# Kernel optimization log

Hardware: AMD Instinct MI355X
Metric: run time of the kernel (lower is better)

## Reference

```python
import jax, jax.numpy as jnp
import numpy as np

N_NODES = 100000


def setup_inputs() -> dict:
    key = jax.random.key(0)
    k1, k2, k3, k4, k5 = jax.random.split(key, 5)
    in_dim, out_dim, n_edges = 128, 128, 640000
    x = jax.random.normal(k1, (N_NODES, in_dim), dtype=jnp.float32)
    src = jax.random.randint(k2, (n_edges,), 0, N_NODES, dtype=jnp.int32)
    dst = jax.random.randint(k3, (n_edges,), 0, N_NODES, dtype=jnp.int32)
    edge_index = jnp.stack([src, dst], axis=0)  # [2, E]
    # nn.Linear default init: U(-1/sqrt(in_dim), 1/sqrt(in_dim))
    bound = 1.0 / np.sqrt(in_dim)
    W = jax.random.uniform(k4, (out_dim, in_dim), minval=-bound, maxval=bound, dtype=jnp.float32)
    b = jax.random.uniform(k5, (out_dim,), minval=-bound, maxval=bound, dtype=jnp.float32)
    return {"x": x, "edge_index": edge_index, "W": W, "b": b}


def reference(x, edge_index, W, b):
    src, dst = edge_index[0], edge_index[1]
    # scatter-sum of gathered source features into destination nodes
    agg = jax.ops.segment_sum(x[src], dst, num_segments=N_NODES)       # [N, d]
    deg = jax.ops.segment_sum(jnp.ones((src.shape[0], 1), x.dtype), dst,
                              num_segments=N_NODES)                     # [N, 1]
    deg = jnp.maximum(deg, 1.0)
    h = agg / deg + x                                                   # mean-agg + residual
    out = jax.nn.relu(h @ W.T + b)                                      # linear + relu (dropout p=0)
    return out
```

## Files before the change

### kernel.cpp

```cpp
#include <hip/hip_runtime.h>
#include <hip/hip_bf16.h>

constexpr int N_NODES = 100000;
constexpr int DIM     = 128;
constexpr int N_EDGES = 640000;

constexpr int CHUNK     = 1024;
constexpr int N_CHUNKS  = (N_NODES + CHUNK - 1) / CHUNK;
constexpr int BINCAP    = 8192;
constexpr int EPB       = 1024;
constexpr int SRC_BITS  = 17;
constexpr int SRC_MASK  = (1 << SRC_BITS) - 1;

constexpr int YNB = 32;

typedef __attribute__((ext_vector_type(4))) float        f32x4;
typedef __attribute__((ext_vector_type(8))) short        bf16x8;
typedef __attribute__((ext_vector_type(4))) unsigned int u32x4;

static __device__ inline unsigned short f2bf(float f) {
    __hip_bfloat16 h = __float2bfloat16(f);
    return *reinterpret_cast<unsigned short*>(&h);
}
static __device__ inline float bf_lo(unsigned u) { return __uint_as_float(u << 16); }
static __device__ inline float bf_hi(unsigned u) { return __uint_as_float(u & 0xffff0000u); }

static __device__ inline bf16x8 pack8(f32x4 a, f32x4 b) {
    bf16x8 v;
    v[0] = (short)f2bf(a.x); v[1] = (short)f2bf(a.y);
    v[2] = (short)f2bf(a.z); v[3] = (short)f2bf(a.w);
    v[4] = (short)f2bf(b.x); v[5] = (short)f2bf(b.y);
    v[6] = (short)f2bf(b.z); v[7] = (short)f2bf(b.w);
    return v;
}

__global__ __launch_bounds__(256) void gcn_gemm_y(
    const float* __restrict__ x,
    const float* __restrict__ W,
    unsigned short* __restrict__ y,
    int* __restrict__ bincur)
{
    __shared__ unsigned short wl[DIM][DIM + 8];

    const int tid = threadIdx.x;
    const int n0  = blockIdx.x * YNB;

    if (blockIdx.x == 0 && tid < 128) bincur[tid] = 0;

    #pragma unroll
    for (int rep = 0; rep < 8; ++rep) {
        const int e   = rep * 2048 + tid * 8;
        const int row = e >> 7;
        const int col = e & 127;
        f32x4 a = *reinterpret_cast<const f32x4*>(W + e);
        f32x4 b = *reinterpret_cast<const f32x4*>(W + e + 4);
        *reinterpret_cast<bf16x8*>(&wl[row][col]) = pack8(a, b);
    }
    __syncthreads();

    const int w    = tid >> 6;
    const int lane = tid & 63;
    const int r    = lane & 15;
    const int g    = lane >> 4;
    const int rowt  = w & 1;
    const int cbase = 4 * (w >> 1);

    bf16x8 af[4];
    #pragma unroll
    for (int t = 0; t < 4; ++t) {
        const float* xp = x + (size_t)(n0 + 16 * rowt + r) * DIM + 32 * t + 8 * g;
        f32x4 a = *reinterpret_cast<const f32x4*>(xp);
        f32x4 b = *reinterpret_cast<const f32x4*>(xp + 4);
        af[t] = pack8(a, b);
    }

    #pragma unroll
    for (int cc = 0; cc < 4; ++cc) {
        const int c = cbase + cc;
        f32x4 acc = {0.f, 0.f, 0.f, 0.f};
        #pragma unroll
        for (int t = 0; t < 4; ++t) {
            bf16x8 wf = *reinterpret_cast<const bf16x8*>(&wl[16 * c + r][32 * t + 8 * g]);
            acc = __builtin_amdgcn_mfma_f32_16x16x32_bf16(af[t], wf, acc, 0, 0, 0);
        }
        #pragma unroll
        for (int q = 0; q < 4; ++q)
            y[(size_t)(n0 + 16 * rowt + 4 * g + q) * DIM + 16 * c + r] =
                f2bf(acc[q]);
    }
}

__global__ __launch_bounds__(256) void gcn_bin(const int* __restrict__ src,
                                               const int* __restrict__ dst,
                                               int* __restrict__ bincur,
                                               unsigned int* __restrict__ bindata)
{
    __shared__ int bh[N_CHUNKS];
    __shared__ int btb[N_CHUNKS];

    const int t  = threadIdx.x;
    const int e0 = blockIdx.x * EPB + t * 4;

    if (t < N_CHUNKS) bh[t] = 0;
    __syncthreads();

    const int4 s4 = *reinterpret_cast<const int4*>(src + e0);
    const int4 d4 = *reinterpret_cast<const int4*>(dst + e0);

    int bin[4], pos[4];
    unsigned pv[4];
    const int ds[4] = {d4.x, d4.y, d4.z, d4.w};
    const int ss[4] = {s4.x, s4.y, s4.z, s4.w};
    #pragma unroll
    for (int q = 0; q < 4; ++q) {
        bin[q] = ds[q] >> 10;
        pv[q]  = (unsigned)ss[q] | ((unsigned)(ds[q] & (CHUNK - 1)) << SRC_BITS);
        pos[q] = atomicAdd(&bh[bin[q]], 1);
    }
    __syncthreads();

    if (t < N_CHUNKS) btb[t] = atomicAdd(&bincur[t], bh[t]);
    __syncthreads();

    #pragma unroll
    for (int q = 0; q < 4; ++q)
        bindata[(size_t)bin[q] * BINCAP + btb[bin[q]] + pos[q]] = pv[q];
}

__global__ __launch_bounds__(256) void gcn_build(const int* __restrict__ bincur,
                                                 unsigned int* __restrict__ bindata,
                                                 int* __restrict__ off)
{
    __shared__ unsigned stage[BINCAP];
    __shared__ int hist[CHUNK];
    __shared__ int s[256];

    const int c  = blockIdx.x;
    const int t  = threadIdx.x;
    const int nb = min(bincur[c], BINCAP);
    unsigned int* region = bindata + (size_t)c * BINCAP;

    for (int e = t; e < nb; e += 256) stage[e] = region[e];
    #pragma unroll
    for (int q = 0; q < 4; ++q) hist[t + 256 * q] = 0;
    __syncthreads();

    for (int e = t; e < nb; e += 256)
        atomicAdd(&hist[stage[e] >> SRC_BITS], 1);
    __syncthreads();

    int h0 = hist[4 * t + 0], h1 = hist[4 * t + 1];
    int h2 = hist[4 * t + 2], h3 = hist[4 * t + 3];
    s[t] = h0 + h1 + h2 + h3;
    __syncthreads();
    for (int d = 1; d < 256; d <<= 1) {
        int add = (t >= d) ? s[t - d] : 0;
        __syncthreads();
        s[t] += add;
        __syncthreads();
    }
    int excl = (t > 0) ? s[t - 1] : 0;

    const int st0 = excl;
    const int st1 = excl + h0;
    const int st2 = excl + h0 + h1;
    const int st3 = excl + h0 + h1 + h2;
    hist[4 * t + 0] = st0;  hist[4 * t + 1] = st1;
    hist[4 * t + 2] = st2;  hist[4 * t + 3] = st3;

    const int nbase = c * CHUNK;
    if (nbase + 4 * t + 0 < N_NODES) off[nbase + 4 * t + 0] = st0 | (h0 << 13);
    if (nbase + 4 * t + 1 < N_NODES) off[nbase + 4 * t + 1] = st1 | (h1 << 13);
    if (nbase + 4 * t + 2 < N_NODES) off[nbase + 4 * t + 2] = st2 | (h2 << 13);
    if (nbase + 4 * t + 3 < N_NODES) off[nbase + 4 * t + 3] = st3 | (h3 << 13);
    __syncthreads();

    for (int e = t; e < nb; e += 256) {
        unsigned v  = stage[e];
        int slot    = atomicAdd(&hist[v >> SRC_BITS], 1);
        region[slot] = v & SRC_MASK;
    }
}

static __device__ inline void acc8(float* acc, u32x4 v) {
    #pragma unroll
    for (int q = 0; q < 4; ++q) {
        unsigned u = v[q];
        acc[2 * q]     += bf_lo(u);
        acc[2 * q + 1] += bf_hi(u);
    }
}

__global__ __launch_bounds__(256) void gcn_agg(
    const unsigned short* __restrict__ y,
    const int* __restrict__ off,
    const unsigned int* __restrict__ csr,
    const float* __restrict__ bias,
    float* __restrict__ out)
{
    const int tid    = threadIdx.x;
    const int lane16 = tid & 15;
    const int n      = blockIdx.x * 16 + (tid >> 4);
    const int col8   = lane16 * 8;

    const int meta  = off[n];
    const int count = meta >> 13;
    int i           = (n >> 10) * BINCAP + (meta & (BINCAP - 1));
    const int end   = i + count;

    float acc[8];
    #pragma unroll
    for (int q = 0; q < 8; ++q) acc[q] = 0.0f;

    for (; i + 4 <= end; i += 4) {
        int s0 = csr[i], s1 = csr[i + 1], s2 = csr[i + 2], s3 = csr[i + 3];
        u32x4 v0 = *reinterpret_cast<const u32x4*>(y + (size_t)s0 * DIM + col8);
        u32x4 v1 = *reinterpret_cast<const u32x4*>(y + (size_t)s1 * DIM + col8);
        u32x4 v2 = *reinterpret_cast<const u32x4*>(y + (size_t)s2 * DIM + col8);
        u32x4 v3 = *reinterpret_cast<const u32x4*>(y + (size_t)s3 * DIM + col8);
        acc8(acc, v0); acc8(acc, v1); acc8(acc, v2); acc8(acc, v3);
    }
    for (; i < end; ++i) {
        u32x4 v = *reinterpret_cast<const u32x4*>(y + (size_t)csr[i] * DIM + col8);
        acc8(acc, v);
    }

    const float inv = 1.0f / fmaxf((float)count, 1.0f);
    const u32x4 yr = *reinterpret_cast<const u32x4*>(y + (size_t)n * DIM + col8);
    const f32x4 b0 = *reinterpret_cast<const f32x4*>(bias + col8);
    const f32x4 b1 = *reinterpret_cast<const f32x4*>(bias + col8 + 4);

    f32x4 o0, o1;
    o0.x = fmaxf(acc[0] * inv + bf_lo(yr[0]) + b0.x, 0.0f);
    o0.y = fmaxf(acc[1] * inv + bf_hi(yr[0]) + b0.y, 0.0f);
    o0.z = fmaxf(acc[2] * inv + bf_lo(yr[1]) + b0.z, 0.0f);
    o0.w = fmaxf(acc[3] * inv + bf_hi(yr[1]) + b0.w, 0.0f);
    o1.x = fmaxf(acc[4] * inv + bf_lo(yr[2]) + b1.x, 0.0f);
    o1.y = fmaxf(acc[5] * inv + bf_hi(yr[2]) + b1.y, 0.0f);
    o1.z = fmaxf(acc[6] * inv + bf_lo(yr[3]) + b1.z, 0.0f);
    o1.w = fmaxf(acc[7] * inv + bf_hi(yr[3]) + b1.w, 0.0f);

    *reinterpret_cast<f32x4*>(out + (size_t)n * DIM + col8)     = o0;
    *reinterpret_cast<f32x4*>(out + (size_t)n * DIM + col8 + 4) = o1;
}

extern "C" void kernel_launch(void* const* d_in, const int* in_sizes, int n_in,
                              void* d_out, int out_size, void* d_ws, size_t ws_size,
                              hipStream_t stream)
{
    const float* x    = (const float*)d_in[0];
    const int*   eidx = (const int*)d_in[1];
    const float* W    = (const float*)d_in[2];
    const float* bias = (const float*)d_in[3];
    float*       out  = (float*)d_out;

    const int* src = eidx;
    const int* dst = eidx + N_EDGES;

    int* bincur = (int*)d_ws;
    int* off    = bincur + 128;
    unsigned int* bindata = (unsigned int*)(off + 100352);
    unsigned short* y = (unsigned short*)(bindata + (size_t)N_CHUNKS * BINCAP);

    gcn_gemm_y<<<N_NODES / YNB, 256, 0, stream>>>(x, W, y, bincur);
    gcn_bin   <<<N_EDGES / EPB, 256, 0, stream>>>(src, dst, bincur, bindata);
    gcn_build <<<N_CHUNKS, 256, 0, stream>>>(bincur, bindata, off);
    gcn_agg   <<<N_NODES / 16, 256, 0, stream>>>(y, off, bindata, bias, out);
}
```

Baseline: 90.85 us.

## Fuse edge binning into GEMM launch and replace global bin atomics with per-block counts

The edge-binning kernel is merged into the GEMM kernel as extra blocks, which removes one launch and lets binning overlap the matrix multiply. Instead of global atomic bin cursors, each bin block writes its edges locally sorted by chunk and records per-chunk counts and offsets. The build kernel prefix-sums those counts and gathers each chunk's edges serially per thread into shared memory. Output stores become nontemporal. The serial per-thread gather in build loads up to about 30 small segments per thread and may be poorly balanced and uncoalesced.

```diff
diff --git a/kernel.cpp b/kernel.cpp
--- a/kernel.cpp
+++ b/kernel.cpp
@@ -12,7 +12,10 @@
 constexpr int SRC_BITS  = 17;
 constexpr int SRC_MASK  = (1 << SRC_BITS) - 1;
 
-constexpr int YNB = 32;
+constexpr int YNB         = 32;
+constexpr int GEMM_BLOCKS = N_NODES / YNB;
+constexpr int BIN_BLOCKS  = N_EDGES / EPB;
+constexpr int DSTRIDE     = 640;
 
 typedef __attribute__((ext_vector_type(4))) float        f32x4;
 typedef __attribute__((ext_vector_type(8))) short        bf16x8;
@@ -34,18 +37,68 @@
     return v;
 }
 
-__global__ __launch_bounds__(256) void gcn_gemm_y(
+__global__ __launch_bounds__(256) void gcn_gemm_bin(
     const float* __restrict__ x,
     const float* __restrict__ W,
+    const int* __restrict__ esrc,
+    const int* __restrict__ edst,
     unsigned short* __restrict__ y,
-    int* __restrict__ bincur)
+    unsigned int* __restrict__ blkdata,
+    int* __restrict__ bcnt,
+    int* __restrict__ bst)
 {
     __shared__ unsigned short wl[DIM][DIM + 8];
+    __shared__ int bh[N_CHUNKS];
+    __shared__ int bpre[128];
 
     const int tid = threadIdx.x;
-    const int n0  = blockIdx.x * YNB;
-
-    if (blockIdx.x == 0 && tid < 128) bincur[tid] = 0;
+
+    if (blockIdx.x >= GEMM_BLOCKS) {
+        const int b  = blockIdx.x - GEMM_BLOCKS;
+        const int e0 = b * EPB + tid * 4;
+
+        if (tid < N_CHUNKS) bh[tid] = 0;
+        __syncthreads();
+
+        const int4 s4 = *reinterpret_cast<const int4*>(esrc + e0);
+        const int4 d4 = *reinterpret_cast<const int4*>(edst + e0);
+        const int ds[4] = {d4.x, d4.y, d4.z, d4.w};
+        const int ss[4] = {s4.x, s4.y, s4.z, s4.w};
+
+        int bin[4], pos[4];
+        unsigned pv[4];
+        #pragma unroll
+        for (int q = 0; q < 4; ++q) {
+            bin[q] = ds[q] >> 10;
+            pv[q]  = (unsigned)ss[q] | ((unsigned)(ds[q] & (CHUNK - 1)) << SRC_BITS);
+            pos[q] = atomicAdd(&bh[bin[q]], 1);
+        }
+        __syncthreads();
+
+        if (tid < 128) bpre[tid] = (tid < N_CHUNKS) ? bh[tid] : 0;
+        __syncthreads();
+        for (int d = 1; d < 128; d <<= 1) {
+            int add = 0;
+            if (tid < 128 && tid >= d) add = bpre[tid - d];
+            __syncthreads();
+            if (tid < 128) bpre[tid] += add;
+            __syncthreads();
+        }
+        if (tid < N_CHUNKS) {
+            bcnt[tid * DSTRIDE + b] = bh[tid];
+            bst [tid * DSTRIDE + b] = (tid > 0) ? bpre[tid - 1] : 0;
+        }
+        __syncthreads();
+
+        #pragma unroll
+        for (int q = 0; q < 4; ++q) {
+            const int excl = (bin[q] > 0) ? bpre[bin[q] - 1] : 0;
+            blkdata[(size_t)b * EPB + excl + pos[q]] = pv[q];
+        }
+        return;
+    }
+
+    const int n0 = blockIdx.x * YNB;
 
     #pragma unroll
     for (int rep = 0; rep < 8; ++rep) {
@@ -90,59 +143,54 @@
     }
 }
 
-__global__ __launch_bounds__(256) void gcn_bin(const int* __restrict__ src,
-                                               const int* __restrict__ dst,
-                                               int* __restrict__ bincur,
-                                               unsigned int* __restrict__ bindata)
-{
-    __shared__ int bh[N_CHUNKS];
-    __shared__ int btb[N_CHUNKS];
-
-    const int t  = threadIdx.x;
-    const int e0 = blockIdx.x * EPB + t * 4;
-
-    if (t < N_CHUNKS) bh[t] = 0;
-    __syncthreads();
-
-    const int4 s4 = *reinterpret_cast<const int4*>(src + e0);
-    const int4 d4 = *reinterpret_cast<const int4*>(dst + e0);
-
-    int bin[4], pos[4];
-    unsigned pv[4];
-    const int ds[4] = {d4.x, d4.y, d4.z, d4.w};
-    const int ss[4] = {s4.x, s4.y, s4.z, s4.w};
-    #pragma unroll
-    for (int q = 0; q < 4; ++q) {
-        bin[q] = ds[q] >> 10;
-        pv[q]  = (unsigned)ss[q] | ((unsigned)(ds[q] & (CHUNK - 1)) << SRC_BITS);
-        pos[q] = atomicAdd(&bh[bin[q]], 1);
-    }
-    __syncthreads();
-
-    if (t < N_CHUNKS) btb[t] = atomicAdd(&bincur[t], bh[t]);
-    __syncthreads();
-
-    #pragma unroll
-    for (int q = 0; q < 4; ++q)
-        bindata[(size_t)bin[q] * BINCAP + btb[bin[q]] + pos[q]] = pv[q];
-}
-
-__global__ __launch_bounds__(256) void gcn_build(const int* __restrict__ bincur,
-                                                 unsigned int* __restrict__ bindata,
-                                                 int* __restrict__ off)
+__global__ __launch_bounds__(256) void gcn_build(
+    const unsigned int* __restrict__ blkdata,
+    const int* __restrict__ bcnt,
+    const int* __restrict__ bst,
+    unsigned int* __restrict__ csr,
+    int* __restrict__ off)
 {
     __shared__ unsigned stage[BINCAP];
     __shared__ int hist[CHUNK];
     __shared__ int s[256];
 
-    const int c  = blockIdx.x;
-    const int t  = threadIdx.x;
-    const int nb = min(bincur[c], BINCAP);
-    unsigned int* region = bindata + (size_t)c * BINCAP;
-
-    for (int e = t; e < nb; e += 256) stage[e] = region[e];
+    const int c = blockIdx.x;
+    const int t = threadIdx.x;
+
     #pragma unroll
     for (int q = 0; q < 4; ++q) hist[t + 256 * q] = 0;
+
+    const int base = t * 3;
+    int v0 = (base + 0 < BIN_BLOCKS) ? bcnt[c * DSTRIDE + base + 0] : 0;
+    int v1 = (base + 1 < BIN_BLOCKS) ? bcnt[c * DSTRIDE + base + 1] : 0;
+    int v2 = (base + 2 < BIN_BLOCKS) ? bcnt[c * DSTRIDE + base + 2] : 0;
+
+    s[t] = v0 + v1 + v2;
+    __syncthreads();
+    for (int d = 1; d < 256; d <<= 1) {
+        int add = (t >= d) ? s[t - d] : 0;
+        __syncthreads();
+        s[t] += add;
+        __syncthreads();
+    }
+    const int nb   = min(s[255], BINCAP);
+    const int excl = (t > 0) ? s[t - 1] : 0;
+
+    {
+        int run = excl;
+        const int vv[3] = {v0, v1, v2};
+        #pragma unroll
+        for (int k = 0; k < 3; ++k) {
+            const int i = base + k;
+            const int n = vv[k];
+            if (i < BIN_BLOCKS && n > 0) {
+                const unsigned* p = blkdata + (size_t)i * EPB + bst[c * DSTRIDE + i];
+                for (int e = 0; e < n; ++e)
+                    if (run + e < BINCAP) stage[run + e] = p[e];
+                run += n;
+            }
+        }
+    }
     __syncthreads();
 
     for (int e = t; e < nb; e += 256)
@@ -159,12 +207,12 @@
         s[t] += add;
         __syncthreads();
     }
-    int excl = (t > 0) ? s[t - 1] : 0;
-
-    const int st0 = excl;
-    const int st1 = excl + h0;
-    const int st2 = excl + h0 + h1;
-    const int st3 = excl + h0 + h1 + h2;
+    int nexcl = (t > 0) ? s[t - 1] : 0;
+
+    const int st0 = nexcl;
+    const int st1 = nexcl + h0;
+    const int st2 = nexcl + h0 + h1;
+    const int st3 = nexcl + h0 + h1 + h2;
     hist[4 * t + 0] = st0;  hist[4 * t + 1] = st1;
     hist[4 * t + 2] = st2;  hist[4 * t + 3] = st3;
 
@@ -176,9 +224,9 @@
     __syncthreads();
 
     for (int e = t; e < nb; e += 256) {
-        unsigned v  = stage[e];
-        int slot    = atomicAdd(&hist[v >> SRC_BITS], 1);
-        region[slot] = v & SRC_MASK;
+        unsigned v = stage[e];
+        int slot   = atomicAdd(&hist[v >> SRC_BITS], 1);
+        csr[(size_t)c * BINCAP + slot] = v & SRC_MASK;
     }
 }
 
@@ -240,8 +288,8 @@
     o1.z = fmaxf(acc[6] * inv + bf_lo(yr[3]) + b1.z, 0.0f);
     o1.w = fmaxf(acc[7] * inv + bf_hi(yr[3]) + b1.w, 0.0f);
 
-    *reinterpret_cast<f32x4*>(out + (size_t)n * DIM + col8)     = o0;
-    *reinterpret_cast<f32x4*>(out + (size_t)n * DIM + col8 + 4) = o1;
+    __builtin_nontemporal_store(o0, reinterpret_cast<f32x4*>(out + (size_t)n * DIM + col8));
+    __builtin_nontemporal_store(o1, reinterpret_cast<f32x4*>(out + (size_t)n * DIM + col8 + 4));
 }
 
 extern "C" void kernel_launch(void* const* d_in, const int* in_sizes, int n_in,
@@ -254,16 +302,18 @@
     const float* bias = (const float*)d_in[3];
     float*       out  = (float*)d_out;
 
-    const int* src = eidx;
-    const int* dst = eidx + N_EDGES;
-
-    int* bincur = (int*)d_ws;
-    int* off    = bincur + 128;
-    unsigned int* bindata = (unsigned int*)(off + 100352);
-    unsigned short* y = (unsigned short*)(bindata + (size_t)N_CHUNKS * BINCAP);
-
-    gcn_gemm_y<<<N_NODES / YNB, 256, 0, stream>>>(x, W, y, bincur);
-    gcn_bin   <<<N_EDGES / EPB, 256, 0, stream>>>(src, dst, bincur, bindata);
-    gcn_build <<<N_CHUNKS, 256, 0, stream>>>(bincur, bindata, off);
-    gcn_agg   <<<N_NODES / 16, 256, 0, stream>>>(y, off, bindata, bias, out);
-}
+    const int* esrc = eidx;
+    const int* edst = eidx + N_EDGES;
+
+    int* bcnt             = (int*)d_ws;
+    int* bst              = bcnt + N_CHUNKS * DSTRIDE;
+    unsigned int* blkdata = (unsigned int*)(bst + N_CHUNKS * DSTRIDE);
+    unsigned int* csr     = blkdata + (size_t)BIN_BLOCKS * EPB;
+    int* off              = (int*)(csr + (size_t)N_CHUNKS * BINCAP);
+    unsigned short* y     = (unsigned short*)(off + 100352);
+
+    gcn_gemm_bin<<<GEMM_BLOCKS + BIN_BLOCKS, 256, 0, stream>>>(
+        x, W, esrc, edst, y, blkdata, bcnt, bst);
+    gcn_build<<<N_CHUNKS, 256, 0, stream>>>(blkdata, bcnt, bst, csr, off);
+    gcn_agg  <<<N_NODES / 16, 256, 0, stream>>>(y, off, csr, bias, out);
+}
```

Result: no change. 91.95 us (+1.2%).
